# Kernel tuning notes

Hardware: AMD Instinct MI355X
Metric: run time of the kernel (lower is better)

## Reference

```python
import jax, jax.numpy as jnp
import numpy as np

NUM_HEADS = 6

def setup_inputs() -> dict:
    key = jax.random.key(0)
    ks = jax.random.split(key, 6)
    B_, N, C = 4096, 64, 192
    nW = 4096
    return {
        "x": jax.random.normal(ks[0], (B_, N, C), dtype=jnp.float32),
        "mask": jax.random.normal(ks[1], (nW, N, N), dtype=jnp.float32),
        "qkv_w": jax.random.normal(ks[2], (3 * C, C), dtype=jnp.float32) * 0.02,
        "qkv_b": jax.random.normal(ks[3], (3 * C,), dtype=jnp.float32) * 0.02,
        "proj_w": jax.random.normal(ks[4], (C, C), dtype=jnp.float32) * 0.02,
        "proj_b": jax.random.normal(ks[5], (C,), dtype=jnp.float32) * 0.02,
    }

def reference(x, mask, qkv_w, qkv_b, proj_w, proj_b):
    B_, N, C = x.shape
    H = NUM_HEADS
    hd = C // H
    scale = hd ** -0.5
    qkv = (x @ qkv_w.T + qkv_b).reshape(B_, N, 3, H, hd)
    qkv = jnp.transpose(qkv, (2, 0, 3, 1, 4))  # [3, B_, H, N, hd]
    q, k, v = qkv[0], qkv[1], qkv[2]
    attn = jnp.einsum('bhnd,bhmd->bhnm', q * scale, k)  # [B_, H, N, N]
    nW = mask.shape[0]
    # additive relative/shift mask broadcast over image batch and heads
    attn = attn.reshape(B_ // nW, nW, H, N, N) + mask[None, :, None, :, :]
    attn = attn.reshape(B_, H, N, N)
    attn = jax.nn.softmax(attn, axis=-1)
    out = jnp.einsum('bhnm,bhmd->bhnd', attn, v)  # [B_, H, N, hd]
    out = jnp.transpose(out, (0, 2, 1, 3)).reshape(B_, N, C)
    return out @ proj_w.T + proj_b
```

## Files before the change

kernel.cpp:

```cpp
#include <hip/hip_runtime.h>
#include <hip/hip_bf16.h>
#include <stdint.h>


#define NTOK 64
#define CDIM 192
#define KROW 40
#define VROW 72
#define CHUNK 3072

typedef __attribute__((ext_vector_type(4))) float f32x4;
typedef __attribute__((ext_vector_type(8))) short bf16x8;

__device__ __forceinline__ short f2bf(float f) {
  __hip_bfloat16 h = __float2bfloat16(f);
  return *reinterpret_cast<short*>(&h);
}
__device__ __forceinline__ uint32_t pack2(float a, float b) {
  __hip_bfloat162 h2;
  h2.x = __float2bfloat16(a);
  h2.y = __float2bfloat16(b);
  return *reinterpret_cast<uint32_t*>(&h2);
}

__device__ __forceinline__ bf16x8 xpose(uint32_t A0, uint32_t A1,
                                        uint32_t B0, uint32_t B1,
                                        int s0, int hiSel) {
  uint32_t w[4];
  uint32_t a, b;
  a = (uint32_t)__shfl((int)A0, s0);      b = (uint32_t)__shfl((int)B0, s0);      w[0] = hiSel ? b : a;
  a = (uint32_t)__shfl((int)A1, s0);      b = (uint32_t)__shfl((int)B1, s0);      w[1] = hiSel ? b : a;
  a = (uint32_t)__shfl((int)A0, s0 + 16); b = (uint32_t)__shfl((int)B0, s0 + 16); w[2] = hiSel ? b : a;
  a = (uint32_t)__shfl((int)A1, s0 + 16); b = (uint32_t)__shfl((int)B1, s0 + 16); w[3] = hiSel ? b : a;
  return *reinterpret_cast<bf16x8*>(w);
}

#define MFMA16(A, B, C) __builtin_amdgcn_mfma_f32_16x16x32_bf16((A), (B), (C), 0, 0, 0)

__device__ __forceinline__ f32x4 gemm6_w_af(const short* __restrict__ p0,
                                            const short* __restrict__ p1,
                                            const bf16x8* __restrict__ af) {
  f32x4 acc = {0.f, 0.f, 0.f, 0.f};
  acc = MFMA16(*reinterpret_cast<const bf16x8*>(p0),       af[0], acc);
  acc = MFMA16(*reinterpret_cast<const bf16x8*>(p1),       af[1], acc);
  acc = MFMA16(*reinterpret_cast<const bf16x8*>(p0 + 64),  af[2], acc);
  acc = MFMA16(*reinterpret_cast<const bf16x8*>(p1 + 64),  af[3], acc);
  acc = MFMA16(*reinterpret_cast<const bf16x8*>(p0 + 128), af[4], acc);
  acc = MFMA16(*reinterpret_cast<const bf16x8*>(p1 + 128), af[5], acc);
  return acc;
}
__device__ __forceinline__ f32x4 gemm6_af_w(const short* __restrict__ p0,
                                            const short* __restrict__ p1,
                                            const bf16x8* __restrict__ af) {
  f32x4 acc = {0.f, 0.f, 0.f, 0.f};
  acc = MFMA16(af[0], *reinterpret_cast<const bf16x8*>(p0),       acc);
  acc = MFMA16(af[1], *reinterpret_cast<const bf16x8*>(p1),       acc);
  acc = MFMA16(af[2], *reinterpret_cast<const bf16x8*>(p0 + 64),  acc);
  acc = MFMA16(af[3], *reinterpret_cast<const bf16x8*>(p1 + 64),  acc);
  acc = MFMA16(af[4], *reinterpret_cast<const bf16x8*>(p0 + 128), acc);
  acc = MFMA16(af[5], *reinterpret_cast<const bf16x8*>(p1 + 128), acc);
  return acc;
}

#define GLOAD16(g, l) __builtin_amdgcn_global_load_lds( \
    (const __attribute__((address_space(1))) void*)(g), \
    (__attribute__((address_space(3))) void*)(l), 16, 0, 0)

__global__ void wconv_kernel(const float* __restrict__ qkv_w,
                             const float* __restrict__ proj_w,
                             short* __restrict__ ws) {
  const int r = blockIdx.x, c = threadIdx.x;
  int chunk, lr;
  float val;
  if (r < 192)      { chunk = r >> 4; lr = r & 15; val = qkv_w[r * CDIM + c]; }
  else if (r < 384) { int q = r - 192; int h = q >> 5; int rr = q & 31;
                      chunk = 12 + 4 * h + (rr >> 4); lr = rr & 15; val = qkv_w[r * CDIM + c]; }
  else if (r < 576) { int q = r - 384; int h = q >> 5; int rr = q & 31;
                      chunk = 14 + 4 * h + (rr >> 4); lr = rr & 15; val = qkv_w[r * CDIM + c]; }
  else              { int q = r - 576; chunk = 36 + (q >> 4); lr = q & 15; val = proj_w[q * CDIM + c]; }
  const int s = c >> 3, lo = c & 7;
  const int sp = (s & 24) | ((s ^ lr) & 7);
  ws[chunk * CHUNK + lr * CDIM + sp * 8 + lo] = f2bf(val);
}

__global__ __launch_bounds__(256, 4)
void winattn_kernel(const float* __restrict__ x, const float* __restrict__ mask,
                    const short* __restrict__ ws,
                    const float* __restrict__ qkv_b, const float* __restrict__ proj_b,
                    float* __restrict__ out) {
  __shared__ __align__(16) short wbA[16 * CDIM];
  __shared__ __align__(16) short wbB[16 * CDIM];
  __shared__ __align__(16) short kh[NTOK * KROW];
  __shared__ __align__(16) short vth[32 * VROW];

  const int b    = blockIdx.x;
  const int tid  = threadIdx.x;
  const int lane = tid & 63;
  const int l16  = lane & 15;
  const int g4   = lane >> 4;
  const int m0   = (tid >> 6) * 16;
  const float scale = 0.17677669529663687f;
  const int s0 = (((2 * g4) & 3) << 4) + l16;
  const int hiSel = g4 >> 1;

  const int t0 = ((g4 ^ l16) & 7) << 3;
  const short* rA0 = wbA + l16 * CDIM + t0;
  const short* rA1 = wbA + l16 * CDIM + (t0 ^ 32);
  const short* rB0 = wbB + l16 * CDIM + t0;
  const short* rB1 = wbB + l16 * CDIM + (t0 ^ 32);
  const short* khr = kh + l16 * KROW + g4 * 8;
  short*       khw = kh + (m0 + l16) * KROW + 4 * g4;
  const short* vtr = vth + l16 * VROW + g4 * 8;
  short*       vtw = vth + l16 * VROW + m0 + 4 * g4;
  const int gofs = (tid >> 6) * 512 + lane * 8;
  const int lofs = (tid >> 6) * 512;
  const bool tail = (tid >> 6) < 2;

  {
    GLOAD16(ws + gofs, wbA + lofs);
    if (tail) GLOAD16(ws + gofs + 2048, wbA + lofs + 2048);
    GLOAD16(ws + CHUNK + gofs, wbB + lofs);
    if (tail) GLOAD16(ws + CHUNK + gofs + 2048, wbB + lofs + 2048);
  }
  const float* xr = x + (size_t)b * (NTOK * CDIM) + (m0 + l16) * CDIM;
  bf16x8 af[6];
  #pragma unroll
  for (int ks = 0; ks < 6; ++ks) {
    const float4 v0 = *reinterpret_cast<const float4*>(xr + ks * 32 + g4 * 8);
    const float4 v1 = *reinterpret_cast<const float4*>(xr + ks * 32 + g4 * 8 + 4);
    uint32_t t[4];
    t[0] = pack2(v0.x, v0.y); t[1] = pack2(v0.z, v0.w);
    t[2] = pack2(v1.x, v1.y); t[3] = pack2(v1.z, v1.w);
    af[ks] = *reinterpret_cast<bf16x8*>(t);
  }
  const float* mrowl = mask + (size_t)b * (NTOK * NTOK) + (m0 + l16) * NTOK;

  __syncthreads();

#define STAGE(dst, cidx) do { \
    GLOAD16(ws + (cidx) * CHUNK + gofs, (dst) + lofs); \
    if (tail) GLOAD16(ws + (cidx) * CHUNK + gofs + 2048, (dst) + lofs + 2048); \
  } while (0)

  bf16x8 aq[6];
  uint32_t ue0 = 0, ue1 = 0;
  #pragma unroll
  for (int c = 0; c < 12; ++c) {
    const bool odd = (c & 1);
    f32x4 acc = odd ? gemm6_w_af(rB0, rB1, af) : gemm6_w_af(rA0, rA1, af);
    const float4 bq = *reinterpret_cast<const float4*>(qkv_b + 16 * c + 4 * g4);
    const uint32_t u0 = pack2((acc[0] + bq.x) * scale, (acc[1] + bq.y) * scale);
    const uint32_t u1 = pack2((acc[2] + bq.z) * scale, (acc[3] + bq.w) * scale);
    if (odd) aq[c >> 1] = xpose(ue0, ue1, u0, u1, s0, hiSel);
    else     { ue0 = u0; ue1 = u1; }
    __syncthreads();
    STAGE(odd ? wbB : wbA, c + 2);
  }

  bf16x8 of[6];
  bf16x8 bpa, bpb;
  float rinvP = 1.f;
  #pragma unroll
  for (int h = 0; h < 6; ++h) {
    const int base = 12 + 4 * h;
    {
      f32x4 acc = gemm6_w_af(rA0, rA1, af);
      const float4 bk4 = *reinterpret_cast<const float4*>(qkv_b + 192 + 32 * h + 4 * g4);
      uint2 kw;
      kw.x = pack2(acc[0] + bk4.x, acc[1] + bk4.y);
      kw.y = pack2(acc[2] + bk4.z, acc[3] + bk4.w);
      *reinterpret_cast<uint2*>(khw) = kw;
    }
    if (h > 0) {
      uint32_t uo[2][2];
      #pragma unroll
      for (int ct2 = 0; ct2 < 2; ++ct2) {
        const short* vb = vtr + ct2 * (16 * VROW);
        f32x4 acc = {0.f, 0.f, 0.f, 0.f};
        acc = MFMA16(*reinterpret_cast<const bf16x8*>(vb),      bpa, acc);
        acc = MFMA16(*reinterpret_cast<const bf16x8*>(vb + 32), bpb, acc);
        uo[ct2][0] = pack2(acc[0] * rinvP, acc[1] * rinvP);
        uo[ct2][1] = pack2(acc[2] * rinvP, acc[3] * rinvP);
      }
      of[h - 1] = xpose(uo[0][0], uo[0][1], uo[1][0], uo[1][1], s0, hiSel);
    }
    __syncthreads();
    STAGE(wbA, base + 2);

    {
      f32x4 acc = gemm6_w_af(rB0, rB1, af);
      const float4 bk4 = *reinterpret_cast<const float4*>(qkv_b + 192 + 32 * h + 16 + 4 * g4);
      uint2 kw;
      kw.x = pack2(acc[0] + bk4.x, acc[1] + bk4.y);
      kw.y = pack2(acc[2] + bk4.z, acc[3] + bk4.w);
      *reinterpret_cast<uint2*>(khw + 16) = kw;
    }
    __syncthreads();
    STAGE(wbB, base + 3);

    float4 mreg[4];
    #pragma unroll
    for (int rt = 0; rt < 4; ++rt)
      mreg[rt] = *reinterpret_cast<const float4*>(mrowl + 16 * rt + 4 * g4);
    {
      f32x4 acc = gemm6_af_w(rA0, rA1, af);
      const float bv = qkv_b[384 + 32 * h + l16];
      uint2 vw;
      vw.x = pack2(acc[0] + bv, acc[1] + bv);
      vw.y = pack2(acc[2] + bv, acc[3] + bv);
      *reinterpret_cast<uint2*>(vtw) = vw;
    }
    {
      float pr[4][4];
      float rmax = -1e30f;
      #pragma unroll
      for (int rt = 0; rt < 4; ++rt) {
        f32x4 z = {0.f, 0.f, 0.f, 0.f};
        f32x4 s = MFMA16(*reinterpret_cast<const bf16x8*>(khr + rt * (16 * KROW)), aq[h], z);
        pr[rt][0] = s[0] + mreg[rt].x; pr[rt][1] = s[1] + mreg[rt].y;
        pr[rt][2] = s[2] + mreg[rt].z; pr[rt][3] = s[3] + mreg[rt].w;
        #pragma unroll
        for (int i = 0; i < 4; ++i) rmax = fmaxf(rmax, pr[rt][i]);
      }
      rmax = fmaxf(rmax, __shfl_xor(rmax, 16));
      rmax = fmaxf(rmax, __shfl_xor(rmax, 32));
      float rsum = 0.f;
      #pragma unroll
      for (int rt = 0; rt < 4; ++rt)
        #pragma unroll
        for (int i = 0; i < 4; ++i) { pr[rt][i] = __expf(pr[rt][i] - rmax); rsum += pr[rt][i]; }
      uint32_t wpk[4][2];
      #pragma unroll
      for (int rt = 0; rt < 4; ++rt) {
        wpk[rt][0] = pack2(pr[rt][0], pr[rt][1]);
        wpk[rt][1] = pack2(pr[rt][2], pr[rt][3]);
      }
      bpa = xpose(wpk[0][0], wpk[0][1], wpk[1][0], wpk[1][1], s0, hiSel);
      bpb = xpose(wpk[2][0], wpk[2][1], wpk[3][0], wpk[3][1], s0, hiSel);
      rsum += __shfl_xor(rsum, 16);
      rsum += __shfl_xor(rsum, 32);
      rinvP = 1.f / rsum;
    }
    __syncthreads();
    STAGE(wbA, h < 5 ? base + 4 : 36);

    {
      f32x4 acc = gemm6_af_w(rB0, rB1, af);
      const float bv = qkv_b[384 + 32 * h + 16 + l16];
      uint2 vw;
      vw.x = pack2(acc[0] + bv, acc[1] + bv);
      vw.y = pack2(acc[2] + bv, acc[3] + bv);
      *reinterpret_cast<uint2*>(vtw + 16 * VROW) = vw;
    }
    __syncthreads();
    STAGE(wbB, h < 5 ? base + 5 : 37);
  }

  float* og = out + (size_t)b * (NTOK * CDIM);
  #pragma unroll
  for (int j = 0; j < 12; ++j) {
    const bool odd = (j & 1);
    if (j == 0) {
      uint32_t uo[2][2];
      #pragma unroll
      for (int ct2 = 0; ct2 < 2; ++ct2) {
        const short* vb = vtr + ct2 * (16 * VROW);
        f32x4 acc = {0.f, 0.f, 0.f, 0.f};
        acc = MFMA16(*reinterpret_cast<const bf16x8*>(vb),      bpa, acc);
        acc = MFMA16(*reinterpret_cast<const bf16x8*>(vb + 32), bpb, acc);
        uo[ct2][0] = pack2(acc[0] * rinvP, acc[1] * rinvP);
        uo[ct2][1] = pack2(acc[2] * rinvP, acc[3] * rinvP);
      }
      of[5] = xpose(uo[0][0], uo[0][1], uo[1][0], uo[1][1], s0, hiSel);
    }
    f32x4 acc = odd ? gemm6_af_w(rB0, rB1, of) : gemm6_af_w(rA0, rA1, of);
    const int cc = 16 * j + l16;
    const float pb = proj_b[cc];
    #pragma unroll
    for (int i = 0; i < 4; ++i)
      og[(m0 + 4 * g4 + i) * CDIM + cc] = acc[i] + pb;
    if (j < 10) {
      __syncthreads();
      STAGE(odd ? wbB : wbA, 38 + j);
    } else if (j == 10) {
      __syncthreads();
    }
  }
#undef STAGE
}

extern "C" void kernel_launch(void* const* d_in, const int* in_sizes, int n_in,
                              void* d_out, int out_size, void* d_ws, size_t ws_size,
                              hipStream_t stream) {
  const float* x      = (const float*)d_in[0];
  const float* mask   = (const float*)d_in[1];
  const float* qkv_w  = (const float*)d_in[2];
  const float* qkv_b  = (const float*)d_in[3];
  const float* proj_w = (const float*)d_in[4];
  const float* proj_b = (const float*)d_in[5];
  float* out = (float*)d_out;

  short* ws = (short*)d_ws;

  wconv_kernel<<<768, 192, 0, stream>>>(qkv_w, proj_w, ws);
  winattn_kernel<<<4096, 256, 0, stream>>>(x, mask, ws, qkv_b, proj_b, out);
}
```

Measured before the change: 210.1 us.

## Replace double-buffered weight staging with four-slot LDS ring and paired prefetch

Replaces the two weight-chunk LDS buffers with a four-slot ring. Two chunks are now prefetched after each barrier, which roughly halves the number of __syncthreads calls in the Q, K/V and projection loops. It also gives each global_load_lds more time to land before its chunk is consumed. In exchange, weight LDS grows from 12 KB to 24 KB per block, which could limit occupancy under the 4-blocks-per-CU launch bound.

```diff
diff --git a/kernel.cpp b/kernel.cpp
--- a/kernel.cpp
+++ b/kernel.cpp
@@ -8,6 +8,7 @@
 #define KROW 40
 #define VROW 72
 #define CHUNK 3072
+#define BUF 3072
 
 typedef __attribute__((ext_vector_type(4))) float f32x4;
 typedef __attribute__((ext_vector_type(8))) short bf16x8;
@@ -38,27 +39,27 @@
 #define MFMA16(A, B, C) __builtin_amdgcn_mfma_f32_16x16x32_bf16((A), (B), (C), 0, 0, 0)
 
 __device__ __forceinline__ f32x4 gemm6_w_af(const short* __restrict__ p0,
-                                            const short* __restrict__ p1,
+                                            const short* __restrict__ p1, int off,
                                             const bf16x8* __restrict__ af) {
   f32x4 acc = {0.f, 0.f, 0.f, 0.f};
-  acc = MFMA16(*reinterpret_cast<const bf16x8*>(p0),       af[0], acc);
-  acc = MFMA16(*reinterpret_cast<const bf16x8*>(p1),       af[1], acc);
-  acc = MFMA16(*reinterpret_cast<const bf16x8*>(p0 + 64),  af[2], acc);
-  acc = MFMA16(*reinterpret_cast<const bf16x8*>(p1 + 64),  af[3], acc);
-  acc = MFMA16(*reinterpret_cast<const bf16x8*>(p0 + 128), af[4], acc);
-  acc = MFMA16(*reinterpret_cast<const bf16x8*>(p1 + 128), af[5], acc);
+  acc = MFMA16(*reinterpret_cast<const bf16x8*>(p0 + off),       af[0], acc);
+  acc = MFMA16(*reinterpret_cast<const bf16x8*>(p1 + off),       af[1], acc);
+  acc = MFMA16(*reinterpret_cast<const bf16x8*>(p0 + off + 64),  af[2], acc);
+  acc = MFMA16(*reinterpret_cast<const bf16x8*>(p1 + off + 64),  af[3], acc);
+  acc = MFMA16(*reinterpret_cast<const bf16x8*>(p0 + off + 128), af[4], acc);
+  acc = MFMA16(*reinterpret_cast<const bf16x8*>(p1 + off + 128), af[5], acc);
   return acc;
 }
 __device__ __forceinline__ f32x4 gemm6_af_w(const short* __restrict__ p0,
-                                            const short* __restrict__ p1,
+                                            const short* __restrict__ p1, int off,
                                             const bf16x8* __restrict__ af) {
   f32x4 acc = {0.f, 0.f, 0.f, 0.f};
-  acc = MFMA16(af[0], *reinterpret_cast<const bf16x8*>(p0),       acc);
-  acc = MFMA16(af[1], *reinterpret_cast<const bf16x8*>(p1),       acc);
-  acc = MFMA16(af[2], *reinterpret_cast<const bf16x8*>(p0 + 64),  acc);
-  acc = MFMA16(af[3], *reinterpret_cast<const bf16x8*>(p1 + 64),  acc);
-  acc = MFMA16(af[4], *reinterpret_cast<const bf16x8*>(p0 + 128), acc);
-  acc = MFMA16(af[5], *reinterpret_cast<const bf16x8*>(p1 + 128), acc);
+  acc = MFMA16(af[0], *reinterpret_cast<const bf16x8*>(p0 + off),       acc);
+  acc = MFMA16(af[1], *reinterpret_cast<const bf16x8*>(p1 + off),       acc);
+  acc = MFMA16(af[2], *reinterpret_cast<const bf16x8*>(p0 + off + 64),  acc);
+  acc = MFMA16(af[3], *reinterpret_cast<const bf16x8*>(p1 + off + 64),  acc);
+  acc = MFMA16(af[4], *reinterpret_cast<const bf16x8*>(p0 + off + 128), acc);
+  acc = MFMA16(af[5], *reinterpret_cast<const bf16x8*>(p1 + off + 128), acc);
   return acc;
 }
 
@@ -88,8 +89,7 @@
                     const short* __restrict__ ws,
                     const float* __restrict__ qkv_b, const float* __restrict__ proj_b,
                     float* __restrict__ out) {
-  __shared__ __align__(16) short wbA[16 * CDIM];
-  __shared__ __align__(16) short wbB[16 * CDIM];
+  __shared__ __align__(16) short wb[4 * BUF];
   __shared__ __align__(16) short kh[NTOK * KROW];
   __shared__ __align__(16) short vth[32 * VROW];
 
@@ -104,24 +104,24 @@
   const int hiSel = g4 >> 1;
 
   const int t0 = ((g4 ^ l16) & 7) << 3;
-  const short* rA0 = wbA + l16 * CDIM + t0;
-  const short* rA1 = wbA + l16 * CDIM + (t0 ^ 32);
-  const short* rB0 = wbB + l16 * CDIM + t0;
-  const short* rB1 = wbB + l16 * CDIM + (t0 ^ 32);
+  const short* rw0 = wb + l16 * CDIM + t0;
+  const short* rw1 = wb + l16 * CDIM + (t0 ^ 32);
   const short* khr = kh + l16 * KROW + g4 * 8;
   short*       khw = kh + (m0 + l16) * KROW + 4 * g4;
   const short* vtr = vth + l16 * VROW + g4 * 8;
   short*       vtw = vth + l16 * VROW + m0 + 4 * g4;
   const int gofs = (tid >> 6) * 512 + lane * 8;
-  const int lofs = (tid >> 6) * 512;
+  short* const lw = wb + (tid >> 6) * 512;
   const bool tail = (tid >> 6) < 2;
 
-  {
-    GLOAD16(ws + gofs, wbA + lofs);
-    if (tail) GLOAD16(ws + gofs + 2048, wbA + lofs + 2048);
-    GLOAD16(ws + CHUNK + gofs, wbB + lofs);
-    if (tail) GLOAD16(ws + CHUNK + gofs + 2048, wbB + lofs + 2048);
-  }
+#define STAGE(cidx) do { \
+    const int _lb = ((cidx) & 3) * BUF; \
+    GLOAD16(ws + (cidx) * CHUNK + gofs, lw + _lb); \
+    if (tail) GLOAD16(ws + (cidx) * CHUNK + gofs + 2048, lw + _lb + 2048); \
+  } while (0)
+
+  STAGE(0); STAGE(1); STAGE(2); STAGE(3);
+
   const float* xr = x + (size_t)b * (NTOK * CDIM) + (m0 + l16) * CDIM;
   bf16x8 af[6];
   #pragma unroll
@@ -137,24 +137,20 @@
 
   __syncthreads();
 
-#define STAGE(dst, cidx) do { \
-    GLOAD16(ws + (cidx) * CHUNK + gofs, (dst) + lofs); \
-    if (tail) GLOAD16(ws + (cidx) * CHUNK + gofs + 2048, (dst) + lofs + 2048); \
-  } while (0)
-
   bf16x8 aq[6];
   uint32_t ue0 = 0, ue1 = 0;
   #pragma unroll
   for (int c = 0; c < 12; ++c) {
-    const bool odd = (c & 1);
-    f32x4 acc = odd ? gemm6_w_af(rB0, rB1, af) : gemm6_w_af(rA0, rA1, af);
+    const int off = (c & 3) * BUF;
+    f32x4 acc = gemm6_w_af(rw0, rw1, off, af);
     const float4 bq = *reinterpret_cast<const float4*>(qkv_b + 16 * c + 4 * g4);
     const uint32_t u0 = pack2((acc[0] + bq.x) * scale, (acc[1] + bq.y) * scale);
     const uint32_t u1 = pack2((acc[2] + bq.z) * scale, (acc[3] + bq.w) * scale);
-    if (odd) aq[c >> 1] = xpose(ue0, ue1, u0, u1, s0, hiSel);
-    else     { ue0 = u0; ue1 = u1; }
-    __syncthreads();
-    STAGE(odd ? wbB : wbA, c + 2);
+    if (c & 1) {
+      aq[c >> 1] = xpose(ue0, ue1, u0, u1, s0, hiSel);
+      __syncthreads();
+      STAGE(c + 3); STAGE(c + 4);
+    } else { ue0 = u0; ue1 = u1; }
   }
 
   bf16x8 of[6];
@@ -162,9 +158,9 @@
   float rinvP = 1.f;
   #pragma unroll
   for (int h = 0; h < 6; ++h) {
-    const int base = 12 + 4 * h;
-    {
-      f32x4 acc = gemm6_w_af(rA0, rA1, af);
+    const int c0 = 12 + 4 * h;
+    {
+      f32x4 acc = gemm6_w_af(rw0, rw1, 0 * BUF, af);
       const float4 bk4 = *reinterpret_cast<const float4*>(qkv_b + 192 + 32 * h + 4 * g4);
       uint2 kw;
       kw.x = pack2(acc[0] + bk4.x, acc[1] + bk4.y);
@@ -184,11 +180,8 @@
       }
       of[h - 1] = xpose(uo[0][0], uo[0][1], uo[1][0], uo[1][1], s0, hiSel);
     }
-    __syncthreads();
-    STAGE(wbA, base + 2);
-
-    {
-      f32x4 acc = gemm6_w_af(rB0, rB1, af);
+    {
+      f32x4 acc = gemm6_w_af(rw0, rw1, 1 * BUF, af);
       const float4 bk4 = *reinterpret_cast<const float4*>(qkv_b + 192 + 32 * h + 16 + 4 * g4);
       uint2 kw;
       kw.x = pack2(acc[0] + bk4.x, acc[1] + bk4.y);
@@ -196,14 +189,14 @@
       *reinterpret_cast<uint2*>(khw + 16) = kw;
     }
     __syncthreads();
-    STAGE(wbB, base + 3);
+    STAGE(c0 + 4); STAGE(c0 + 5);
 
     float4 mreg[4];
     #pragma unroll
     for (int rt = 0; rt < 4; ++rt)
       mreg[rt] = *reinterpret_cast<const float4*>(mrowl + 16 * rt + 4 * g4);
     {
-      f32x4 acc = gemm6_af_w(rA0, rA1, af);
+      f32x4 acc = gemm6_af_w(rw0, rw1, 2 * BUF, af);
       const float bv = qkv_b[384 + 32 * h + l16];
       uint2 vw;
       vw.x = pack2(acc[0] + bv, acc[1] + bv);
@@ -241,11 +234,8 @@
       rsum += __shfl_xor(rsum, 32);
       rinvP = 1.f / rsum;
     }
-    __syncthreads();
-    STAGE(wbA, h < 5 ? base + 4 : 36);
-
-    {
-      f32x4 acc = gemm6_af_w(rB0, rB1, af);
+    {
+      f32x4 acc = gemm6_af_w(rw0, rw1, 3 * BUF, af);
       const float bv = qkv_b[384 + 32 * h + 16 + l16];
       uint2 vw;
       vw.x = pack2(acc[0] + bv, acc[1] + bv);
@@ -253,13 +243,14 @@
       *reinterpret_cast<uint2*>(vtw + 16 * VROW) = vw;
     }
     __syncthreads();
-    STAGE(wbB, h < 5 ? base + 5 : 37);
+    STAGE(c0 + 6); STAGE(c0 + 7);
   }
 
   float* og = out + (size_t)b * (NTOK * CDIM);
   #pragma unroll
   for (int j = 0; j < 12; ++j) {
-    const bool odd = (j & 1);
+    const int c = 36 + j;
+    const int off = (c & 3) * BUF;
     if (j == 0) {
       uint32_t uo[2][2];
       #pragma unroll
@@ -273,17 +264,16 @@
       }
       of[5] = xpose(uo[0][0], uo[0][1], uo[1][0], uo[1][1], s0, hiSel);
     }
-    f32x4 acc = odd ? gemm6_af_w(rB0, rB1, of) : gemm6_af_w(rA0, rA1, of);
+    f32x4 acc = gemm6_af_w(rw0, rw1, off, of);
     const int cc = 16 * j + l16;
     const float pb = proj_b[cc];
     #pragma unroll
     for (int i = 0; i < 4; ++i)
       og[(m0 + 4 * g4 + i) * CDIM + cc] = acc[i] + pb;
-    if (j < 10) {
+    if ((j & 1) && j < 11) {
       __syncthreads();
-      STAGE(odd ? wbB : wbA, 38 + j);
-    } else if (j == 10) {
-      __syncthreads();
+      if (c + 3 < 48) { STAGE(c + 3); STAGE(c + 4); }
+      else if (c + 3 == 48 - 1 + 1) {  }
     }
   }
 #undef STAGE
```

After: 209.3 us. About the same (-0.4%).
